# Kernel tuning notes

Hardware: AMD Instinct MI355X
Metric: run time of the kernel (lower is better)

The kernel has to match this reference:

```python
import jax, jax.numpy as jnp
import numpy as np

LOG2 = 0.6931471805599453  # shifted_softplus(x) = softplus(x) - log(2)
NUM_MOL = 20_000  # static maxm for segment reduction


def ssp(x):
    return jax.nn.softplus(x) - LOG2


def setup_inputs() -> dict:
    key = jax.random.key(0)
    ks = jax.random.split(key, 5)
    N, D, H, E, M = 1_000_000, 128, 64, 4, NUM_MOL
    x = jax.random.normal(ks[0], (N, D), dtype=jnp.float32)
    zidx = jax.random.randint(ks[1], (N,), 0, E, dtype=jnp.int32)
    idx_m = jnp.sort(jax.random.randint(ks[2], (N,), 0, M, dtype=jnp.int32))
    # stacked per-element pyramidal MLP params: D -> D//2 -> 1
    W1 = jax.random.normal(ks[3], (E, D, H), dtype=jnp.float32) * (1.0 / np.sqrt(D))
    b1 = jnp.zeros((E, H), dtype=jnp.float32)
    W2 = jax.random.normal(ks[4], (E, H, 1), dtype=jnp.float32) * (1.0 / np.sqrt(H))
    b2 = jnp.zeros((E, 1), dtype=jnp.float32)
    return dict(x=x, zidx=zidx, idx_m=idx_m, W1=W1, b1=b1, W2=W2, b2=b2)


def reference(x, zidx, idx_m, W1, b1, W2, b2):
    # ElementwiseMLP: run each element's 2-layer MLP, select per atom by element.
    E = W1.shape[0]
    yi = jnp.zeros((x.shape[0], W2.shape[-1]), dtype=x.dtype)  # [N, n_out]
    for e in range(E):  # small fixed element set
        h = ssp(x @ W1[e] + b1[e])            # [N, H]
        ye = h @ W2[e] + b2[e]                # [N, n_out]
        yi = yi + jnp.where((zidx == e)[:, None], ye, jnp.zeros((), dtype=x.dtype))
    # aggregation_mode == 'sum': index_add per molecule
    y = jax.ops.segment_sum(yi, idx_m, num_segments=NUM_MOL)  # [M, n_out]
    return jnp.squeeze(y, -1)  # [M]
```

## Files before the change

kernel.cpp:

```cpp
#include <hip/hip_runtime.h>

typedef _Float16 half8 __attribute__((ext_vector_type(8)));
typedef float f32x4 __attribute__((ext_vector_type(4)));

#define LDSROW 136

__global__ __launch_bounds__(256, 2)
void elemental_atomwise_kernel(const float* __restrict__ x,
                               const int* __restrict__ zidx,
                               const int* __restrict__ idx_m,
                               const float* __restrict__ W1,
                               const float* __restrict__ b1,
                               const float* __restrict__ W2,
                               const float* __restrict__ b2,
                               float* __restrict__ y,
                               int N) {
  extern __shared__ _Float16 w1t[];

#pragma unroll
  for (int it = 0; it < 32; ++it) {
    int idx4 = threadIdx.x + it * 256;
    f32x4 v = ((const f32x4*)W1)[idx4];
    int lin = idx4 << 2;
    int e = lin >> 13;
    int d = (lin >> 6) & 127;
    int h = lin & 63;
    int n = e * 64 + h;
#pragma unroll
    for (int j = 0; j < 4; ++j)
      w1t[(n + j) * LDSROW + d] = (_Float16)v[j];
  }
  __syncthreads();

  const int lane = threadIdx.x & 63;
  const int wave = threadIdx.x >> 6;
  const int c = lane & 15;
  const int q = lane >> 4;
  const long tile = (long)blockIdx.x * 4 + wave;
  const long base = tile * 64;
  if (base >= N) return;

  int ameta = (base + lane < N) ? (int)(base + lane) : (N - 1);
  const int zvec = zidx[ameta];
  const int ivec = idx_m[ameta];

  half8 af[4][4];
#pragma unroll
  for (int mt = 0; mt < 4; ++mt) {
    long row = base + mt * 16 + c;
    if (row >= N) row = N - 1;
    const f32x4* rp = (const f32x4*)(x + row * 128);
#pragma unroll
    for (int kt = 0; kt < 4; ++kt) {
      f32x4 u0 = rp[kt * 8 + q * 2];
      f32x4 u1 = rp[kt * 8 + q * 2 + 1];
      half8 a;
      a[0] = (_Float16)u0[0]; a[1] = (_Float16)u0[1];
      a[2] = (_Float16)u0[2]; a[3] = (_Float16)u0[3];
      a[4] = (_Float16)u1[0]; a[5] = (_Float16)u1[1];
      a[6] = (_Float16)u1[2]; a[7] = (_Float16)u1[3];
      af[mt][kt] = a;
    }
  }

#pragma unroll
  for (int e = 0; e < 4; ++e) {
    f32x4 acc[4][4];
#pragma unroll
    for (int mt = 0; mt < 4; ++mt)
#pragma unroll
      for (int nt = 0; nt < 4; ++nt)
        acc[mt][nt] = (f32x4){0.f, 0.f, 0.f, 0.f};

#pragma unroll
    for (int kt = 0; kt < 4; ++kt) {
#pragma unroll
      for (int nt = 0; nt < 4; ++nt) {
        half8 bf = *(const half8*)&w1t[(e * 64 + nt * 16 + c) * LDSROW + kt * 32 + q * 8];
#pragma unroll
        for (int mt = 0; mt < 4; ++mt)
          acc[mt][nt] = __builtin_amdgcn_mfma_f32_16x16x32_f16(af[mt][kt], bf, acc[mt][nt], 0, 0, 0);
      }
    }

    float b1v[4], w2v[4];
#pragma unroll
    for (int nt = 0; nt < 4; ++nt) {
      b1v[nt] = b1[e * 64 + nt * 16 + c];
      w2v[nt] = W2[e * 64 + nt * 16 + c];
    }
    const float b2e = b2[e];
#pragma unroll
    for (int mt = 0; mt < 4; ++mt) {
#pragma unroll
      for (int i = 0; i < 4; ++i) {
        float s = 0.0f;
#pragma unroll
        for (int nt = 0; nt < 4; ++nt) {
          float t = acc[mt][nt][i] + b1v[nt];
          float hsp = __logf(1.0f + __expf(t)) - 0.69314718056f;
          s = fmaf(hsp, w2v[nt], s);
        }
        s += __shfl_xor(s, 1);
        s += __shfl_xor(s, 2);
        s += __shfl_xor(s, 4);
        s += __shfl_xor(s, 8);
        int mloc = mt * 16 + q * 4 + i;
        int zm = __shfl(zvec, mloc);
        int im = __shfl(ivec, mloc);
        if (c == 0 && zm == e && base + mloc < N)
          atomicAdd(&y[im], s + b2e);
      }
    }
  }
}

extern "C" void kernel_launch(void* const* d_in, const int* in_sizes, int n_in,
                              void* d_out, int out_size, void* d_ws, size_t ws_size,
                              hipStream_t stream) {
  const float* x = (const float*)d_in[0];
  const int* zidx = (const int*)d_in[1];
  const int* idx_m = (const int*)d_in[2];
  const float* W1 = (const float*)d_in[3];
  const float* b1 = (const float*)d_in[4];
  const float* W2 = (const float*)d_in[5];
  const float* b2 = (const float*)d_in[6];
  float* y = (float*)d_out;

  const int N = in_sizes[0] / 128;

  hipMemsetAsync(d_out, 0, (size_t)out_size * sizeof(float), stream);

  const int tiles = (N + 63) / 64;
  const int blocks = (tiles + 3) / 4;
  const size_t lds_bytes = 256 * LDSROW * sizeof(_Float16);

  elemental_atomwise_kernel<<<blocks, 256, lds_bytes, stream>>>(
      x, zidx, idx_m, W1, b1, W2, b2, y, N);
}
```

Measured before the change: 839.4 us.

## Bucket atoms by element and run only the matching expert MLP

Adds count, offset and scatter kernels that build a per-element permutation of atoms in workspace, padded to 256-atom blocks. The main kernel then handles one element per block, loading only that element's W1 into LDS and computing a single expert's matmul and softplus instead of all four. This removes the redundant compute for the other three experts, at the cost of gathered row reads of x, extra small launches, and an atomic-based permutation build. The old kernel remains as a fallback when the workspace is too small.

After: 779.9 us. 7.1% less time.

```diff
diff --git a/kernel.cpp b/kernel.cpp
--- a/kernel.cpp
+++ b/kernel.cpp
@@ -3,7 +3,195 @@
 typedef _Float16 half8 __attribute__((ext_vector_type(8)));
 typedef float f32x4 __attribute__((ext_vector_type(4)));
 
-#define LDSROW 136
+#define WS_COUNT(e)  ((e) * 32)
+#define WS_AOFF(e)   (128 + (e))
+#define WS_FILL(e)   (136 + (e))
+#define WS_CUR(e)    (160 + (e) * 32)
+#define WS_PERM      512
+
+__global__ void k_count(const int* __restrict__ zidx, int N, int* __restrict__ ws) {
+  __shared__ int lh[4];
+  if (threadIdx.x < 4) lh[threadIdx.x] = 0;
+  __syncthreads();
+  const int i = blockIdx.x * 256 + threadIdx.x;
+  const int z = (i < N) ? zidx[i] : -1;
+  const int lane = threadIdx.x & 63;
+#pragma unroll
+  for (int e = 0; e < 4; ++e) {
+    unsigned long long m = __ballot(z == e);
+    if (lane == 0 && m) atomicAdd(&lh[e], __popcll(m));
+  }
+  __syncthreads();
+  if (threadIdx.x < 4 && lh[threadIdx.x])
+    atomicAdd(&ws[WS_COUNT(threadIdx.x)], lh[threadIdx.x]);
+}
+
+__global__ void k_offsets(int* __restrict__ ws) {
+  if (threadIdx.x != 0) return;
+  int off = 0;
+#pragma unroll
+  for (int e = 0; e < 4; ++e) {
+    int c = ws[WS_COUNT(e)];
+    ws[WS_AOFF(e)] = off;
+    ws[WS_FILL(e)] = off + c;
+    ws[WS_CUR(e)] = off;
+    off += (c + 255) & ~255;
+  }
+  ws[WS_AOFF(4)] = off;
+}
+
+__global__ void k_scatter(const int* __restrict__ zidx, int N, int* __restrict__ ws) {
+  __shared__ int wcnt[4][4];
+  __shared__ int wbase[4][4];
+  const int tid = threadIdx.x;
+  const int lane = tid & 63;
+  const int wave = tid >> 6;
+  const int i = blockIdx.x * 256 + tid;
+  const int z = (i < N) ? zidx[i] : -1;
+  const unsigned long long m0 = __ballot(z == 0);
+  const unsigned long long m1 = __ballot(z == 1);
+  const unsigned long long m2 = __ballot(z == 2);
+  const unsigned long long m3 = __ballot(z == 3);
+  if (lane == 0) {
+    wcnt[wave][0] = __popcll(m0);
+    wcnt[wave][1] = __popcll(m1);
+    wcnt[wave][2] = __popcll(m2);
+    wcnt[wave][3] = __popcll(m3);
+  }
+  __syncthreads();
+  if (tid < 4) {
+    const int e = tid;
+    const int c0 = wcnt[0][e], c1 = wcnt[1][e], c2 = wcnt[2][e], c3 = wcnt[3][e];
+    const int base = atomicAdd(&ws[WS_CUR(e)], c0 + c1 + c2 + c3);
+    wbase[0][e] = base;
+    wbase[1][e] = base + c0;
+    wbase[2][e] = base + c0 + c1;
+    wbase[3][e] = base + c0 + c1 + c2;
+  }
+  __syncthreads();
+  if (z >= 0) {
+    const unsigned long long below = (1ull << lane) - 1ull;
+    int r, b;
+    if (z == 0)      { r = __popcll(m0 & below); b = wbase[wave][0]; }
+    else if (z == 1) { r = __popcll(m1 & below); b = wbase[wave][1]; }
+    else if (z == 2) { r = __popcll(m2 & below); b = wbase[wave][2]; }
+    else             { r = __popcll(m3 & below); b = wbase[wave][3]; }
+    ws[WS_PERM + b + r] = i;
+  }
+}
+
+__global__ __launch_bounds__(256, 3)
+void elemental_sorted_kernel(const float* __restrict__ x,
+                             const int* __restrict__ idx_m,
+                             const float* __restrict__ W1,
+                             const float* __restrict__ b1,
+                             const float* __restrict__ W2,
+                             const float* __restrict__ b2,
+                             const int* __restrict__ ws,
+                             float* __restrict__ y) {
+  __shared__ _Float16 w1t[8192];
+
+  const int bstart = blockIdx.x << 8;
+  if (bstart >= ws[WS_AOFF(4)]) return;
+  int e = 0;
+  if (bstart >= ws[WS_AOFF(1)]) e = 1;
+  if (bstart >= ws[WS_AOFF(2)]) e = 2;
+  if (bstart >= ws[WS_AOFF(3)]) e = 3;
+  const int fillE = ws[WS_FILL(e)];
+
+  const float* w1e = W1 + (size_t)e * 8192;
+  const int tid = threadIdx.x;
+#pragma unroll
+  for (int t = 0; t < 4; ++t) {
+    const int ch = tid + t * 256;
+    const int kt = ch >> 8;
+    const int nt = (ch >> 6) & 3;
+    const int l2 = ch & 63;
+    const int h = nt * 16 + (l2 & 15);
+    const int d0 = kt * 32 + (l2 >> 4) * 8;
+    half8 hv;
+#pragma unroll
+    for (int j = 0; j < 8; ++j)
+      hv[j] = (_Float16)w1e[(d0 + j) * 64 + h];
+    *(half8*)&w1t[ch * 8] = hv;
+  }
+  __syncthreads();
+
+  const int lane = tid & 63;
+  const int wave = tid >> 6;
+  const int c = lane & 15;
+  const int q = lane >> 4;
+  const int pos = bstart + wave * 64 + lane;
+  const int ap = (pos < fillE) ? ws[WS_PERM + pos] : -1;
+  const int iv = (ap >= 0) ? idx_m[ap] : 0;
+
+  half8 af[4][4];
+#pragma unroll
+  for (int mt = 0; mt < 4; ++mt) {
+    int pa = __shfl(ap, mt * 16 + c);
+    const f32x4* rp = (const f32x4*)(x + (long)(pa < 0 ? 0 : pa) * 128);
+#pragma unroll
+    for (int kt = 0; kt < 4; ++kt) {
+      f32x4 u0 = rp[kt * 8 + q * 2];
+      f32x4 u1 = rp[kt * 8 + q * 2 + 1];
+      half8 a;
+      a[0] = (_Float16)u0[0]; a[1] = (_Float16)u0[1];
+      a[2] = (_Float16)u0[2]; a[3] = (_Float16)u0[3];
+      a[4] = (_Float16)u1[0]; a[5] = (_Float16)u1[1];
+      a[6] = (_Float16)u1[2]; a[7] = (_Float16)u1[3];
+      af[mt][kt] = a;
+    }
+  }
+
+  f32x4 acc[4][4];
+#pragma unroll
+  for (int mt = 0; mt < 4; ++mt)
+#pragma unroll
+    for (int nt = 0; nt < 4; ++nt)
+      acc[mt][nt] = (f32x4){0.f, 0.f, 0.f, 0.f};
+
+#pragma unroll
+  for (int kt = 0; kt < 4; ++kt)
+#pragma unroll
+    for (int nt = 0; nt < 4; ++nt) {
+      half8 bf = *(const half8*)&w1t[((kt * 4 + nt) * 64 + lane) * 8];
+#pragma unroll
+      for (int mt = 0; mt < 4; ++mt)
+        acc[mt][nt] = __builtin_amdgcn_mfma_f32_16x16x32_f16(af[mt][kt], bf, acc[mt][nt], 0, 0, 0);
+    }
+
+  float b1v[4], w2v[4];
+#pragma unroll
+  for (int nt = 0; nt < 4; ++nt) {
+    b1v[nt] = b1[e * 64 + nt * 16 + c];
+    w2v[nt] = W2[e * 64 + nt * 16 + c];
+  }
+  const float b2e = b2[e];
+#pragma unroll
+  for (int mt = 0; mt < 4; ++mt) {
+#pragma unroll
+    for (int i = 0; i < 4; ++i) {
+      float s = 0.0f;
+#pragma unroll
+      for (int nt = 0; nt < 4; ++nt) {
+        float tv = acc[mt][nt][i] + b1v[nt];
+        float hsp = __logf(1.0f + __expf(tv)) - 0.69314718056f;
+        s = fmaf(hsp, w2v[nt], s);
+      }
+      s += __shfl_xor(s, 1);
+      s += __shfl_xor(s, 2);
+      s += __shfl_xor(s, 4);
+      s += __shfl_xor(s, 8);
+      const int mloc = mt * 16 + q * 4 + i;
+      const int av = __shfl(ap, mloc);
+      const int im = __shfl(iv, mloc);
+      if (c == 0 && av >= 0)
+        atomicAdd(&y[im], s + b2e);
+    }
+  }
+}
+
+#define LDSROW_OLD 136
 
 __global__ __launch_bounds__(256, 2)
 void elemental_atomwise_kernel(const float* __restrict__ x,
@@ -16,19 +204,18 @@
                                float* __restrict__ y,
                                int N) {
   extern __shared__ _Float16 w1t[];
-
 #pragma unroll
   for (int it = 0; it < 32; ++it) {
     int idx4 = threadIdx.x + it * 256;
     f32x4 v = ((const f32x4*)W1)[idx4];
     int lin = idx4 << 2;
-    int e = lin >> 13;
     int d = (lin >> 6) & 127;
+    int ee = lin >> 13;
     int h = lin & 63;
-    int n = e * 64 + h;
+    int n = ee * 64 + h;
 #pragma unroll
     for (int j = 0; j < 4; ++j)
-      w1t[(n + j) * LDSROW + d] = (_Float16)v[j];
+      w1t[(n + j) * LDSROW_OLD + d] = (_Float16)v[j];
   }
   __syncthreads();
 
@@ -76,7 +263,7 @@
     for (int kt = 0; kt < 4; ++kt) {
 #pragma unroll
       for (int nt = 0; nt < 4; ++nt) {
-        half8 bf = *(const half8*)&w1t[(e * 64 + nt * 16 + c) * LDSROW + kt * 32 + q * 8];
+        half8 bf = *(const half8*)&w1t[(e * 64 + nt * 16 + c) * LDSROW_OLD + kt * 32 + q * 8];
 #pragma unroll
         for (int mt = 0; mt < 4; ++mt)
           acc[mt][nt] = __builtin_amdgcn_mfma_f32_16x16x32_f16(af[mt][kt], bf, acc[mt][nt], 0, 0, 0);
@@ -97,8 +284,8 @@
         float s = 0.0f;
 #pragma unroll
         for (int nt = 0; nt < 4; ++nt) {
-          float t = acc[mt][nt][i] + b1v[nt];
-          float hsp = __logf(1.0f + __expf(t)) - 0.69314718056f;
+          float tv = acc[mt][nt][i] + b1v[nt];
+          float hsp = __logf(1.0f + __expf(tv)) - 0.69314718056f;
           s = fmaf(hsp, w2v[nt], s);
         }
         s += __shfl_xor(s, 1);
@@ -131,10 +318,21 @@
 
   hipMemsetAsync(d_out, 0, (size_t)out_size * sizeof(float), stream);
 
-  const int tiles = (N + 63) / 64;
-  const int blocks = (tiles + 3) / 4;
-  const size_t lds_bytes = 256 * LDSROW * sizeof(_Float16);
-
-  elemental_atomwise_kernel<<<blocks, 256, lds_bytes, stream>>>(
-      x, zidx, idx_m, W1, b1, W2, b2, y, N);
-}
+  const size_t ws_need = (size_t)(WS_PERM + N + 1024) * sizeof(int);
+  if (ws_size >= ws_need) {
+    int* ws = (int*)d_ws;
+    hipMemsetAsync(d_ws, 0, 1024, stream);
+    const int nb = (N + 255) / 256;
+    k_count<<<nb, 256, 0, stream>>>(zidx, N, ws);
+    k_offsets<<<1, 64, 0, stream>>>(ws);
+    k_scatter<<<nb, 256, 0, stream>>>(zidx, N, ws);
+    const int nb4 = (N + 1020 + 255) / 256;
+    elemental_sorted_kernel<<<nb4, 256, 0, stream>>>(x, idx_m, W1, b1, W2, b2, ws, y);
+  } else {
+    const int tiles = (N + 63) / 64;
+    const int blocks = (tiles + 3) / 4;
+    const size_t lds_bytes = 256 * LDSROW_OLD * sizeof(_Float16);
+    elemental_atomwise_kernel<<<blocks, 256, lds_bytes, stream>>>(
+        x, zidx, idx_m, W1, b1, W2, b2, y, N);
+  }
+}
```
